# Optimization experiments

Hardware: AMD Instinct MI355X
Metric: run time of the kernel (lower is better)

## Reference

```python
import jax, jax.numpy as jnp
import numpy as np

EMBED = 1024
NUM_EXPERTS = 8
ACTIVE = 2
HIDDEN = 4 * EMBED


def setup_inputs() -> dict:
    key = jax.random.key(0)
    ks = jax.random.split(key, 7)
    B, T = 4, 1024
    s1 = 1.0 / np.sqrt(EMBED)
    s2 = 1.0 / np.sqrt(HIDDEN)
    return {
        "x": jax.random.normal(ks[0], (B, T, EMBED), dtype=jnp.float32),
        # stacked expert weights, layout [in, out] (torch Linear applies x @ W.T + b)
        "W1": jax.random.uniform(ks[1], (NUM_EXPERTS, EMBED, HIDDEN), jnp.float32, -s1, s1),
        "b1": jax.random.uniform(ks[2], (NUM_EXPERTS, HIDDEN), jnp.float32, -s1, s1),
        "W2": jax.random.uniform(ks[3], (NUM_EXPERTS, HIDDEN, EMBED), jnp.float32, -s2, s2),
        "b2": jax.random.uniform(ks[4], (NUM_EXPERTS, EMBED), jnp.float32, -s2, s2),
        "Wr": jax.random.uniform(ks[5], (EMBED, NUM_EXPERTS), jnp.float32, -s1, s1),
        "br": jax.random.uniform(ks[6], (NUM_EXPERTS,), jnp.float32, -s1, s1),
    }


def reference(x, W1, b1, W2, b2, Wr, br):
    # ---- router (TopkRouter) ----
    scores = x @ Wr + br                                  # [B,T,E]
    topk_scores, indices = jax.lax.top_k(scores, ACTIVE)  # [B,T,K]
    # mask = zeros scattered with topk scores at topk positions (others stay 0),
    # then softmax over ALL experts (faithful to the reference's quirky softmax).
    one_hot = jax.nn.one_hot(indices, NUM_EXPERTS, dtype=scores.dtype)  # [B,T,K,E]
    mask = jnp.einsum('btke,btk->bte', one_hot, topk_scores)            # [B,T,E]
    router_output = jax.nn.softmax(mask, axis=-1)                       # [B,T,E]

    # ---- dense all-experts FFN (Expert): relu(x@W1+b1)@W2+b2 per expert ----
    h = jax.nn.relu(jnp.einsum('btd,edh->bteh', x, W1) + b1)            # [B,T,E,H]
    expert_outputs = jnp.einsum('bteh,ehd->bted', h, W2) + b2           # [B,T,E,D]

    # ---- weighted combine ----
    return jnp.einsum('bte,bted->btd', router_output, expert_outputs)   # [B,T,D]
```

## Files before the change

kernel.cpp:

```cpp
#include <hip/hip_runtime.h>
#include <hip/hip_bf16.h>
#include <cstdint>
#include <cstddef>

#define EMBED  1024
#define NEXP   8
#define HIDDEN 4096
#define TOKENS 4096

typedef __attribute__((ext_vector_type(8))) short bf16x8;
typedef __attribute__((ext_vector_type(4))) float f32x4;
using bf16 = __hip_bfloat16;

__device__ __forceinline__ void gload_lds16(const void* g, void* l) {
    __builtin_amdgcn_global_load_lds((const __attribute__((address_space(1))) void*)g,
                                     (__attribute__((address_space(3))) void*)l,
                                     16, 0, 0);
}

__device__ __forceinline__ int swz(int b) { return b ^ (((b >> 7) & 7) << 4); }

__global__ void cvt_kernel(const float* __restrict__ in, bf16* __restrict__ out, size_t n) {
    size_t i = ((size_t)blockIdx.x * blockDim.x + threadIdx.x) * 4;
    if (i + 3 < n) {
        float4 v = *(const float4*)(in + i);
        out[i + 0] = __float2bfloat16(v.x);
        out[i + 1] = __float2bfloat16(v.y);
        out[i + 2] = __float2bfloat16(v.z);
        out[i + 3] = __float2bfloat16(v.w);
    }
}

__global__ void transpose_cvt(const float* __restrict__ in, bf16* __restrict__ out,
                              int K, int N, size_t in_estride, size_t out_eoff, int ldo) {
    const int e = blockIdx.z;
    const float* ine = in + (size_t)e * in_estride;
    bf16* oute = out + (size_t)e * out_eoff;
    __shared__ float tile[32][33];
    const int n0 = blockIdx.x * 32, k0 = blockIdx.y * 32;
    const int tx = threadIdx.x, ty = threadIdx.y;
    #pragma unroll
    for (int i = ty; i < 32; i += 8)
        tile[i][tx] = ine[(size_t)(k0 + i) * N + n0 + tx];
    __syncthreads();
    #pragma unroll
    for (int i = ty; i < 32; i += 8)
        oute[(size_t)(n0 + i) * ldo + k0 + tx] = __float2bfloat16(tile[tx][i]);
}

__global__ void router_kernel(const float* __restrict__ x, const float* __restrict__ Wr,
                              const float* __restrict__ br, float* __restrict__ w) {
    const int t = blockIdx.x;
    const int lane = threadIdx.x;
    const float* xt = x + (size_t)t * EMBED;
    float s[NEXP];
    #pragma unroll
    for (int e = 0; e < NEXP; e++) s[e] = 0.f;
    for (int k = lane; k < EMBED; k += 64) {
        const float xv = xt[k];
        const float* wrk = Wr + (size_t)k * NEXP;
        #pragma unroll
        for (int e = 0; e < NEXP; e++) s[e] = fmaf(xv, wrk[e], s[e]);
    }
    #pragma unroll
    for (int e = 0; e < NEXP; e++) {
        #pragma unroll
        for (int off = 32; off >= 1; off >>= 1)
            s[e] += __shfl_xor(s[e], off);
    }
    if (lane == 0) {
        float sc[NEXP];
        #pragma unroll
        for (int e = 0; e < NEXP; e++) sc[e] = s[e] + br[e];
        int i1 = 0; float m1 = sc[0];
        #pragma unroll
        for (int e = 1; e < NEXP; e++) if (sc[e] > m1) { m1 = sc[e]; i1 = e; }
        int i2 = -1; float m2 = -1e30f;
        #pragma unroll
        for (int e = 0; e < NEXP; e++) if (e != i1 && sc[e] > m2) { m2 = sc[e]; i2 = e; }
        const float mx = fmaxf(m1, 0.f);
        const float denom = 6.f * expf(0.f - mx) + expf(m1 - mx) + expf(m2 - mx);
        #pragma unroll
        for (int e = 0; e < NEXP; e++) {
            float v = (e == i1) ? m1 : ((e == i2) ? m2 : 0.f);
            w[(size_t)t * NEXP + e] = expf(v - mx) / denom;
        }
    }
}


#define BARX()  { __builtin_amdgcn_sched_barrier(0); __builtin_amdgcn_s_barrier(); __builtin_amdgcn_sched_barrier(0); }
#define LGKM0() { asm volatile("s_waitcnt lgkmcnt(0)" ::: "memory"); __builtin_amdgcn_sched_barrier(0); }

#define PIPE_PREAMBLE(Abase, Bbase, lda, ldb)                                        \
    __shared__ __align__(16) bf16 As[2][2][128 * 64];                                \
    __shared__ __align__(16) bf16 Bs[2][2][128 * 64];                                \
    const int tid = threadIdx.x;                                                     \
    const int lane = tid & 63, wid = tid >> 6;                                       \
    const int mhalf = wid >> 2, wB = wid & 3;                                        \
    const int nhalf = wB >> 1, nsub = wB & 1;                                        \
    const int wv_r = mhalf * 128, wv_c = wB * 64;                                    \
    f32x4 acc[8][4] = {};                                                            \
    int rowloc[2], colel[2];                                                         \
    _Pragma("unroll")                                                                \
    for (int j = 0; j < 2; j++) {                                                    \
        int bs = swz(tid * 16 + j * 8192);                                           \
        rowloc[j] = bs >> 7; colel[j] = (bs & 127) >> 1;                             \
    }                                                                                \
    const bf16* pA0 = (Abase) + (size_t)(brow + rowloc[0]) * (lda) + colel[0];       \
    const bf16* pA1 = (Abase) + (size_t)(brow + rowloc[1]) * (lda) + colel[1];       \
    const bf16* pB0 = (Bbase) + (size_t)(bcol + rowloc[0]) * (ldb) + colel[0];       \
    const bf16* pB1 = (Bbase) + (size_t)(bcol + rowloc[1]) * (ldb) + colel[1];       \
    const int fr = lane & 15, kb0 = (lane >> 4) * 16;                                \
    const int xm = (fr & 7) << 4;                                                    \
    const int baA0 = (fr * 128 + kb0) ^ xm, baA1 = (fr * 128 + kb0 + 64) ^ xm;       \
    const int brB = (nsub * 64 + fr) * 128;                                          \
    const int baB0 = (brB + kb0) ^ xm, baB1 = (brB + kb0 + 64) ^ xm;

#define STAGE_A(bi, h, koff, lda)                                                    \
    do {                                                                             \
        gload_lds16(pA0 + (size_t)(h) * 128 * (lda) + (koff), &As[bi][h][tid * 8]);  \
        gload_lds16(pA1 + (size_t)(h) * 128 * (lda) + (koff), &As[bi][h][tid * 8 + 4096]); \
    } while (0)
#define STAGE_B(bi, h, koff, ldb)                                                    \
    do {                                                                             \
        gload_lds16(pB0 + (size_t)(h) * 128 * (ldb) + (koff), &Bs[bi][h][tid * 8]);  \
        gload_lds16(pB1 + (size_t)(h) * 128 * (ldb) + (koff), &Bs[bi][h][tid * 8 + 4096]); \
    } while (0)

#define MFMA_Q(mh, nh)                                                               \
    __builtin_amdgcn_s_setprio(1);                                                   \
    _Pragma("unroll")                                                                \
    for (int mm = 0; mm < 4; mm++)                                                   \
        _Pragma("unroll")                                                            \
        for (int nn = 0; nn < 2; nn++) {                                             \
            acc[(mh)*4+mm][(nh)*2+nn] = __builtin_amdgcn_mfma_f32_16x16x32_bf16(     \
                a[(mh)*4+mm][0], b[(nh)*2+nn][0], acc[(mh)*4+mm][(nh)*2+nn], 0,0,0); \
            acc[(mh)*4+mm][(nh)*2+nn] = __builtin_amdgcn_mfma_f32_16x16x32_bf16(     \
                a[(mh)*4+mm][1], b[(nh)*2+nn][1], acc[(mh)*4+mm][(nh)*2+nn], 0,0,0); \
        }                                                                            \
    __builtin_amdgcn_s_setprio(0);

#define PIPE_KLOOP(NT, lda, ldb)                                                     \
    STAGE_A(0, 0, 0, lda); STAGE_A(0, 1, 0, lda);                                    \
    STAGE_B(0, 0, 0, ldb); STAGE_B(0, 1, 0, ldb);                                    \
    STAGE_A(1, 0, 64, lda); STAGE_A(1, 1, 64, lda);                                  \
    STAGE_B(1, 0, 64, ldb); STAGE_B(1, 1, 64, ldb);                                  \
    asm volatile("s_waitcnt vmcnt(8)" ::: "memory");                                 \
    BARX();                                                                          \
    for (int t = 0; t < (NT); ++t) {                                                 \
        const int bi = t & 1;                                                        \
        const bool st = (t + 2) < (NT);                                              \
        const size_t koff = (size_t)(t + 2) * 64;                                    \
        const char* Ah = (const char*)&As[bi][mhalf][0];                             \
        const char* Bh = (const char*)&Bs[bi][nhalf][0];                             \
        bf16x8 a[8][2], b[4][2];                                                     \
                             \
        _Pragma("unroll")                                                            \
        for (int m = 0; m < 4; m++) {                                                \
            a[m][0] = *(const bf16x8*)(Ah + baA0 + m * 2048);                        \
            a[m][1] = *(const bf16x8*)(Ah + baA1 + m * 2048);                        \
        }                                                                            \
        _Pragma("unroll")                                                            \
        for (int n = 0; n < 2; n++) {                                                \
            b[n][0] = *(const bf16x8*)(Bh + baB0 + n * 2048);                        \
            b[n][1] = *(const bf16x8*)(Bh + baB1 + n * 2048);                        \
        }                                                                            \
        BARX(); LGKM0();                                                             \
        MFMA_Q(0, 0)                                                                 \
        BARX();                                                                      \
                             \
        _Pragma("unroll")                                                            \
        for (int m = 4; m < 8; m++) {                                                \
            a[m][0] = *(const bf16x8*)(Ah + baA0 + m * 2048);                        \
            a[m][1] = *(const bf16x8*)(Ah + baA1 + m * 2048);                        \
        }                                                                            \
        _Pragma("unroll")                                                            \
        for (int n = 2; n < 4; n++) {                                                \
            b[n][0] = *(const bf16x8*)(Bh + baB0 + n * 2048);                        \
            b[n][1] = *(const bf16x8*)(Bh + baB1 + n * 2048);                        \
        }                                                                            \
        BARX(); LGKM0();                                                             \
        MFMA_Q(0, 1)                                                                 \
        BARX();                                                                      \
                \
        if (st) { STAGE_A(bi, 0, koff, lda); STAGE_A(bi, 1, koff, lda); }            \
        MFMA_Q(1, 0)                                                                 \
        BARX();                                                                      \
                      \
        if (st) { STAGE_B(bi, 0, koff, ldb); STAGE_B(bi, 1, koff, ldb); }            \
        MFMA_Q(1, 1)                                                                 \
        if (st) { asm volatile("s_waitcnt vmcnt(8)" ::: "memory"); }                 \
        else    { asm volatile("s_waitcnt vmcnt(0)" ::: "memory"); }                 \
        BARX();                                                                      \
    }

__global__ __launch_bounds__(512, 2) void gemm1(const bf16* __restrict__ A,
                                                const bf16* __restrict__ Bt,
                                                const float* __restrict__ b1,
                                                const float* __restrict__ rw,
                                                bf16* __restrict__ H) {
    const int e = blockIdx.z;
    const int brow = blockIdx.y * 256;
    const int bcol = blockIdx.x * 256;
    const bf16* Be = Bt + (size_t)e * HIDDEN * EMBED;
    bf16* He = H + (size_t)e * TOKENS * HIDDEN;

    PIPE_PREAMBLE(A, Be, EMBED, EMBED)
    PIPE_KLOOP(16, EMBED, EMBED)

    #pragma unroll
    for (int n = 0; n < 4; n++) {
        const int col = bcol + wv_c + n * 16 + fr;
        const float bias = b1[e * HIDDEN + col];
        #pragma unroll
        for (int m = 0; m < 8; m++) {
            const int rowb = brow + wv_r + m * 16 + (lane >> 4) * 4;
            #pragma unroll
            for (int j = 0; j < 4; j++) {
                const int row = rowb + j;
                float v = acc[m][n][j] + bias;
                v = fmaxf(v, 0.f) * rw[(size_t)row * NEXP + e];
                He[(size_t)row * HIDDEN + col] = __float2bfloat16(v);
            }
        }
    }
}

__global__ __launch_bounds__(512, 2) void gemm2(const bf16* __restrict__ A,
                                                const bf16* __restrict__ Bt,
                                                const float* __restrict__ b2,
                                                const float* __restrict__ rw,
                                                float* __restrict__ out) {
    const int e = blockIdx.z;
    const int brow = blockIdx.y * 256;
    const int bcol = blockIdx.x * 256;
    const bf16* Ae = A + (size_t)e * TOKENS * HIDDEN;
    const bf16* Be = Bt + (size_t)e * EMBED * HIDDEN;

    PIPE_PREAMBLE(Ae, Be, HIDDEN, HIDDEN)
    PIPE_KLOOP(64, HIDDEN, HIDDEN)

    #pragma unroll
    for (int n = 0; n < 4; n++) {
        const int col = bcol + wv_c + n * 16 + fr;
        #pragma unroll
        for (int m = 0; m < 8; m++) {
            const int rowb = brow + wv_r + m * 16 + (lane >> 4) * 4;
            #pragma unroll
            for (int j = 0; j < 4; j++) {
                const int row = rowb + j;
                float v = acc[m][n][j];
                if (e == 0) {
                    const float* wrow = rw + (size_t)row * NEXP;
                    float s = 0.f;
                    #pragma unroll
                    for (int ee = 0; ee < NEXP; ee++) s = fmaf(wrow[ee], b2[ee * EMBED + col], s);
                    v += s;
                }
                atomicAdd(out + (size_t)row * EMBED + col, v);
            }
        }
    }
}

extern "C" void kernel_launch(void* const* d_in, const int* in_sizes, int n_in,
                              void* d_out, int out_size, void* d_ws, size_t ws_size,
                              hipStream_t stream) {
    const float* x  = (const float*)d_in[0];
    const float* W1 = (const float*)d_in[1];
    const float* b1 = (const float*)d_in[2];
    const float* W2 = (const float*)d_in[3];
    const float* b2 = (const float*)d_in[4];
    const float* Wr = (const float*)d_in[5];
    const float* br = (const float*)d_in[6];
    float* out = (float*)d_out;

    uint8_t* ws = (uint8_t*)d_ws;
    size_t off = 0;
    auto walloc = [&](size_t bytes) -> void* {
        void* p = ws + off;
        off += (bytes + 255) & ~(size_t)255;
        return p;
    };
    float* rw  = (float*)walloc((size_t)TOKENS * NEXP * 4);
    bf16* xb   = (bf16*)walloc((size_t)TOKENS * EMBED * 2);
    bf16* w1t  = (bf16*)walloc((size_t)NEXP * HIDDEN * EMBED * 2);
    bf16* w2t  = (bf16*)walloc((size_t)NEXP * EMBED * HIDDEN * 2);
    bf16* hbuf = (bf16*)walloc((size_t)NEXP * TOKENS * HIDDEN * 2);

    hipMemsetAsync(d_out, 0, (size_t)out_size * sizeof(float), stream);

    cvt_kernel<<<4096, 256, 0, stream>>>(x, xb, (size_t)TOKENS * EMBED);

    dim3 tb(32, 8);
    transpose_cvt<<<dim3(HIDDEN / 32, EMBED / 32, NEXP), tb, 0, stream>>>(
        W1, w1t, EMBED, HIDDEN, (size_t)EMBED * HIDDEN, (size_t)HIDDEN * EMBED, EMBED);
    transpose_cvt<<<dim3(EMBED / 32, HIDDEN / 32, NEXP), tb, 0, stream>>>(
        W2, w2t, HIDDEN, EMBED, (size_t)HIDDEN * EMBED, (size_t)EMBED * HIDDEN, HIDDEN);

    router_kernel<<<TOKENS, 64, 0, stream>>>(x, Wr, br, rw);

    gemm1<<<dim3(HIDDEN / 256, TOKENS / 256, NEXP), 512, 0, stream>>>(xb, w1t, b1, rw, hbuf);
    gemm2<<<dim3(EMBED / 256, TOKENS / 256, NEXP), 512, 0, stream>>>(hbuf, w2t, b2, rw, out);
}
```

Before: 950.6 us.

## Replace gemm1 with simple 128x128 tile kernel and reorder gemm2 pipeline stages

```diff
diff --git a/kernel.cpp b/kernel.cpp
--- a/kernel.cpp
+++ b/kernel.cpp
@@ -84,6 +84,70 @@
         for (int e = 0; e < NEXP; e++) {
             float v = (e == i1) ? m1 : ((e == i2) ? m2 : 0.f);
             w[(size_t)t * NEXP + e] = expf(v - mx) / denom;
+        }
+    }
+}
+
+__global__ __launch_bounds__(256) void gemm1(const bf16* __restrict__ A,
+                                             const bf16* __restrict__ Bt,
+                                             const float* __restrict__ b1,
+                                             const float* __restrict__ rw,
+                                             bf16* __restrict__ H) {
+    const int e = blockIdx.z;
+    const int brow = blockIdx.y * 128;
+    const int bcol = blockIdx.x * 128;
+    const bf16* Be = Bt + (size_t)e * HIDDEN * EMBED;
+    bf16* He = H + (size_t)e * TOKENS * HIDDEN;
+    __shared__ __align__(16) bf16 As[128 * 32];
+    __shared__ __align__(16) bf16 Bs[128 * 32];
+    const int tid = threadIdx.x;
+    f32x4 acc[4][4] = {};
+
+    const int seg0 = tid, seg1 = tid + 256;
+    const int r0 = seg0 >> 2, c0 = seg0 & 3;
+    const int r1 = seg1 >> 2, c1 = seg1 & 3;
+    const bf16* ga0 = A + (size_t)(brow + r0) * EMBED + c0 * 8;
+    const bf16* ga1 = A + (size_t)(brow + r1) * EMBED + c1 * 8;
+    const bf16* gb0 = Be + (size_t)(bcol + r0) * EMBED + c0 * 8;
+    const bf16* gb1 = Be + (size_t)(bcol + r1) * EMBED + c1 * 8;
+
+    const int lane = tid & 63, wid = tid >> 6;
+    const int wv_r = (wid >> 1) * 64, wv_c = (wid & 1) * 64;
+    const int fr = lane & 15, kb = (lane >> 4) * 8;
+
+    for (int kt = 0; kt < EMBED; kt += 32) {
+        gload_lds16(ga0 + kt, As + seg0 * 8);
+        gload_lds16(ga1 + kt, As + seg1 * 8);
+        gload_lds16(gb0 + kt, Bs + seg0 * 8);
+        gload_lds16(gb1 + kt, Bs + seg1 * 8);
+        __syncthreads();
+        bf16x8 af[4], bfr[4];
+        #pragma unroll
+        for (int m = 0; m < 4; m++) af[m] = *(const bf16x8*)&As[(wv_r + m * 16 + fr) * 32 + kb];
+        #pragma unroll
+        for (int n = 0; n < 4; n++) bfr[n] = *(const bf16x8*)&Bs[(wv_c + n * 16 + fr) * 32 + kb];
+        #pragma unroll
+        for (int m = 0; m < 4; m++)
+            #pragma unroll
+            for (int n = 0; n < 4; n++)
+                acc[m][n] = __builtin_amdgcn_mfma_f32_16x16x32_bf16(af[m], bfr[n], acc[m][n], 0, 0, 0);
+        __syncthreads();
+    }
+
+    #pragma unroll
+    for (int n = 0; n < 4; n++) {
+        const int col = bcol + wv_c + n * 16 + fr;
+        const float bias = b1[e * HIDDEN + col];
+        #pragma unroll
+        for (int m = 0; m < 4; m++) {
+            const int rowb = brow + wv_r + m * 16 + (lane >> 4) * 4;
+            #pragma unroll
+            for (int j = 0; j < 4; j++) {
+                const int row = rowb + j;
+                float v = acc[m][n][j] + bias;
+                v = fmaxf(v, 0.f) * rw[(size_t)row * NEXP + e];
+                He[(size_t)row * HIDDEN + col] = __float2bfloat16(v);
+            }
         }
     }
 }
@@ -155,7 +219,7 @@
         const char* Ah = (const char*)&As[bi][mhalf][0];                             \
         const char* Bh = (const char*)&Bs[bi][nhalf][0];                             \
         bf16x8 a[8][2], b[4][2];                                                     \
-                             \
+                                        \
         _Pragma("unroll")                                                            \
         for (int m = 0; m < 4; m++) {                                                \
             a[m][0] = *(const bf16x8*)(Ah + baA0 + m * 2048);                        \
@@ -168,64 +232,32 @@
         }                                                                            \
         BARX(); LGKM0();                                                             \
         MFMA_Q(0, 0)                                                                 \
+             \
+        _Pragma("unroll")                                                            \
+        for (int n = 2; n < 4; n++) {                                                \
+            b[n][0] = *(const bf16x8*)(Bh + baB0 + n * 2048);                        \
+            b[n][1] = *(const bf16x8*)(Bh + baB1 + n * 2048);                        \
+        }                                                                            \
+        BARX(); LGKM0();                                                             \
+        MFMA_Q(0, 1)                                                                 \
         BARX();                                                                      \
-                             \
+           \
         _Pragma("unroll")                                                            \
         for (int m = 4; m < 8; m++) {                                                \
             a[m][0] = *(const bf16x8*)(Ah + baA0 + m * 2048);                        \
             a[m][1] = *(const bf16x8*)(Ah + baA1 + m * 2048);                        \
         }                                                                            \
-        _Pragma("unroll")                                                            \
-        for (int n = 2; n < 4; n++) {                                                \
-            b[n][0] = *(const bf16x8*)(Bh + baB0 + n * 2048);                        \
-            b[n][1] = *(const bf16x8*)(Bh + baB1 + n * 2048);                        \
-        }                                                                            \
+        if (st) { STAGE_B(bi, 0, koff, ldb); STAGE_B(bi, 1, koff, ldb); }            \
         BARX(); LGKM0();                                                             \
-        MFMA_Q(0, 1)                                                                 \
-        BARX();                                                                      \
-                \
-        if (st) { STAGE_A(bi, 0, koff, lda); STAGE_A(bi, 1, koff, lda); }            \
         MFMA_Q(1, 0)                                                                 \
         BARX();                                                                      \
-                      \
-        if (st) { STAGE_B(bi, 0, koff, ldb); STAGE_B(bi, 1, koff, ldb); }            \
+             \
+        if (st) { STAGE_A(bi, 0, koff, lda); STAGE_A(bi, 1, koff, lda); }            \
         MFMA_Q(1, 1)                                                                 \
         if (st) { asm volatile("s_waitcnt vmcnt(8)" ::: "memory"); }                 \
         else    { asm volatile("s_waitcnt vmcnt(0)" ::: "memory"); }                 \
         BARX();                                                                      \
     }
-
-__global__ __launch_bounds__(512, 2) void gemm1(const bf16* __restrict__ A,
-                                                const bf16* __restrict__ Bt,
-                                                const float* __restrict__ b1,
-                                                const float* __restrict__ rw,
-                                                bf16* __restrict__ H) {
-    const int e = blockIdx.z;
-    const int brow = blockIdx.y * 256;
-    const int bcol = blockIdx.x * 256;
-    const bf16* Be = Bt + (size_t)e * HIDDEN * EMBED;
-    bf16* He = H + (size_t)e * TOKENS * HIDDEN;
-
-    PIPE_PREAMBLE(A, Be, EMBED, EMBED)
-    PIPE_KLOOP(16, EMBED, EMBED)
-
-    #pragma unroll
-    for (int n = 0; n < 4; n++) {
-        const int col = bcol + wv_c + n * 16 + fr;
-        const float bias = b1[e * HIDDEN + col];
-        #pragma unroll
-        for (int m = 0; m < 8; m++) {
-            const int rowb = brow + wv_r + m * 16 + (lane >> 4) * 4;
-            #pragma unroll
-            for (int j = 0; j < 4; j++) {
-                const int row = rowb + j;
-                float v = acc[m][n][j] + bias;
-                v = fmaxf(v, 0.f) * rw[(size_t)row * NEXP + e];
-                He[(size_t)row * HIDDEN + col] = __float2bfloat16(v);
-            }
-        }
-    }
-}
 
 __global__ __launch_bounds__(512, 2) void gemm2(const bf16* __restrict__ A,
                                                 const bf16* __restrict__ Bt,
@@ -301,6 +333,6 @@
 
     router_kernel<<<TOKENS, 64, 0, stream>>>(x, Wr, br, rw);
 
-    gemm1<<<dim3(HIDDEN / 256, TOKENS / 256, NEXP), 512, 0, stream>>>(xb, w1t, b1, rw, hbuf);
+    gemm1<<<dim3(HIDDEN / 128, TOKENS / 128, NEXP), 256, 0, stream>>>(xb, w1t, b1, rw, hbuf);
     gemm2<<<dim3(EMBED / 256, TOKENS / 256, NEXP), 512, 0, stream>>>(hbuf, w2t, b2, rw, out);
 }
```

Result: no change. 941.5 us (-1.0%).

## Replace gemm2 fp32 atomics with per-expert-pair partials and a reduce kernel

Applied to the files above, without the earlier changes.

```diff
diff --git a/kernel.cpp b/kernel.cpp
--- a/kernel.cpp
+++ b/kernel.cpp
@@ -18,7 +18,7 @@
                                      16, 0, 0);
 }
 
-__device__ __forceinline__ int swz(int b) { return b ^ (((b >> 7) & 7) << 4); }
+__device__ __forceinline__ int swzB(int b) { return b ^ (((b >> 7) & 7) << 4); }
 
 __global__ void cvt_kernel(const float* __restrict__ in, bf16* __restrict__ out, size_t n) {
     size_t i = ((size_t)blockIdx.x * blockDim.x + threadIdx.x) * 4;
@@ -88,9 +88,40 @@
     }
 }
 
+__global__ __launch_bounds__(256) void reduce_kernel(const float* __restrict__ p,
+                                                     const float* __restrict__ rw,
+                                                     const float* __restrict__ b2,
+                                                     float* __restrict__ out) {
+    const int row = blockIdx.x;
+    const int c4 = threadIdx.x * 4;
+    const size_t S = (size_t)TOKENS * EMBED;
+    const float* pr = p + (size_t)row * EMBED + c4;
+    float4 v0 = *(const float4*)(pr);
+    float4 v1 = *(const float4*)(pr + S);
+    float4 v2 = *(const float4*)(pr + 2 * S);
+    float4 v3 = *(const float4*)(pr + 3 * S);
+    float4 v;
+    v.x = v0.x + v1.x + v2.x + v3.x;
+    v.y = v0.y + v1.y + v2.y + v3.y;
+    v.z = v0.z + v1.z + v2.z + v3.z;
+    v.w = v0.w + v1.w + v2.w + v3.w;
+    const float* wrow = rw + (size_t)row * NEXP;
+    #pragma unroll
+    for (int e = 0; e < NEXP; e++) {
+        const float we = wrow[e];
+        float4 bb = *(const float4*)(b2 + (size_t)e * EMBED + c4);
+        v.x = fmaf(we, bb.x, v.x);
+        v.y = fmaf(we, bb.y, v.y);
+        v.z = fmaf(we, bb.z, v.z);
+        v.w = fmaf(we, bb.w, v.w);
+    }
+    *(float4*)(out + (size_t)row * EMBED + c4) = v;
+}
 
 #define BARX()  { __builtin_amdgcn_sched_barrier(0); __builtin_amdgcn_s_barrier(); __builtin_amdgcn_sched_barrier(0); }
 #define LGKM0() { asm volatile("s_waitcnt lgkmcnt(0)" ::: "memory"); __builtin_amdgcn_sched_barrier(0); }
+
+#define KOFF(T, estride) ((size_t)((T) & 63) * 64 + (size_t)((T) >> 6) * (estride))
 
 #define PIPE_PREAMBLE(Abase, Bbase, lda, ldb)                                        \
     __shared__ __align__(16) bf16 As[2][2][128 * 64];                                \
@@ -104,7 +135,7 @@
     int rowloc[2], colel[2];                                                         \
     _Pragma("unroll")                                                                \
     for (int j = 0; j < 2; j++) {                                                    \
-        int bs = swz(tid * 16 + j * 8192);                                           \
+        int bs = swzB(tid * 16 + j * 8192);                                          \
         rowloc[j] = bs >> 7; colel[j] = (bs & 127) >> 1;                             \
     }                                                                                \
     const bf16* pA0 = (Abase) + (size_t)(brow + rowloc[0]) * (lda) + colel[0];       \
@@ -141,7 +172,7 @@
         }                                                                            \
     __builtin_amdgcn_s_setprio(0);
 
-#define PIPE_KLOOP(NT, lda, ldb)                                                     \
+#define PIPE_KLOOP(NT, lda, ldb, eA, eB)                                             \
     STAGE_A(0, 0, 0, lda); STAGE_A(0, 1, 0, lda);                                    \
     STAGE_B(0, 0, 0, ldb); STAGE_B(0, 1, 0, ldb);                                    \
     STAGE_A(1, 0, 64, lda); STAGE_A(1, 1, 64, lda);                                  \
@@ -151,11 +182,12 @@
     for (int t = 0; t < (NT); ++t) {                                                 \
         const int bi = t & 1;                                                        \
         const bool st = (t + 2) < (NT);                                              \
-        const size_t koff = (size_t)(t + 2) * 64;                                    \
+        const size_t koffA = KOFF(t + 2, eA);                                        \
+        const size_t koffB = KOFF(t + 2, eB);                                        \
         const char* Ah = (const char*)&As[bi][mhalf][0];                             \
         const char* Bh = (const char*)&Bs[bi][nhalf][0];                             \
         bf16x8 a[8][2], b[4][2];                                                     \
-                             \
+                                        \
         _Pragma("unroll")                                                            \
         for (int m = 0; m < 4; m++) {                                                \
             a[m][0] = *(const bf16x8*)(Ah + baA0 + m * 2048);                        \
@@ -168,27 +200,27 @@
         }                                                                            \
         BARX(); LGKM0();                                                             \
         MFMA_Q(0, 0)                                                                 \
+                                                   \
+        _Pragma("unroll")                                                            \
+        for (int n = 2; n < 4; n++) {                                                \
+            b[n][0] = *(const bf16x8*)(Bh + baB0 + n * 2048);                        \
+            b[n][1] = *(const bf16x8*)(Bh + baB1 + n * 2048);                        \
+        }                                                                            \
+        BARX(); LGKM0();                                                             \
+        MFMA_Q(0, 1)                                                                 \
         BARX();                                                                      \
-                             \
+                                     \
         _Pragma("unroll")                                                            \
         for (int m = 4; m < 8; m++) {                                                \
             a[m][0] = *(const bf16x8*)(Ah + baA0 + m * 2048);                        \
             a[m][1] = *(const bf16x8*)(Ah + baA1 + m * 2048);                        \
         }                                                                            \
-        _Pragma("unroll")                                                            \
-        for (int n = 2; n < 4; n++) {                                                \
-            b[n][0] = *(const bf16x8*)(Bh + baB0 + n * 2048);                        \
-            b[n][1] = *(const bf16x8*)(Bh + baB1 + n * 2048);                        \
-        }                                                                            \
+        if (st) { STAGE_B(bi, 0, koffB, ldb); STAGE_B(bi, 1, koffB, ldb); }          \
         BARX(); LGKM0();                                                             \
-        MFMA_Q(0, 1)                                                                 \
-        BARX();                                                                      \
-                \
-        if (st) { STAGE_A(bi, 0, koff, lda); STAGE_A(bi, 1, koff, lda); }            \
         MFMA_Q(1, 0)                                                                 \
         BARX();                                                                      \
-                      \
-        if (st) { STAGE_B(bi, 0, koff, ldb); STAGE_B(bi, 1, koff, ldb); }            \
+                       \
+        if (st) { STAGE_A(bi, 0, koffA, lda); STAGE_A(bi, 1, koffA, lda); }          \
         MFMA_Q(1, 1)                                                                 \
         if (st) { asm volatile("s_waitcnt vmcnt(8)" ::: "memory"); }                 \
         else    { asm volatile("s_waitcnt vmcnt(0)" ::: "memory"); }                 \
@@ -207,7 +239,7 @@
     bf16* He = H + (size_t)e * TOKENS * HIDDEN;
 
     PIPE_PREAMBLE(A, Be, EMBED, EMBED)
-    PIPE_KLOOP(16, EMBED, EMBED)
+    PIPE_KLOOP(16, EMBED, EMBED, (size_t)0, (size_t)0)
 
     #pragma unroll
     for (int n = 0; n < 4; n++) {
@@ -229,17 +261,18 @@
 
 __global__ __launch_bounds__(512, 2) void gemm2(const bf16* __restrict__ A,
                                                 const bf16* __restrict__ Bt,
-                                                const float* __restrict__ b2,
-                                                const float* __restrict__ rw,
-                                                float* __restrict__ out) {
-    const int e = blockIdx.z;
+                                                float* __restrict__ partials) {
+    const int kc = blockIdx.z;
     const int brow = blockIdx.y * 256;
     const int bcol = blockIdx.x * 256;
-    const bf16* Ae = A + (size_t)e * TOKENS * HIDDEN;
-    const bf16* Be = Bt + (size_t)e * EMBED * HIDDEN;
+    const size_t eA = (size_t)TOKENS * HIDDEN;
+    const size_t eB = (size_t)EMBED * HIDDEN;
+    const bf16* Ae = A + (size_t)(kc * 2) * eA;
+    const bf16* Be = Bt + (size_t)(kc * 2) * eB;
+    float* pout = partials + (size_t)kc * TOKENS * EMBED;
 
     PIPE_PREAMBLE(Ae, Be, HIDDEN, HIDDEN)
-    PIPE_KLOOP(64, HIDDEN, HIDDEN)
+    PIPE_KLOOP(128, HIDDEN, HIDDEN, eA, eB)
 
     #pragma unroll
     for (int n = 0; n < 4; n++) {
@@ -250,15 +283,7 @@
             #pragma unroll
             for (int j = 0; j < 4; j++) {
                 const int row = rowb + j;
-                float v = acc[m][n][j];
-                if (e == 0) {
-                    const float* wrow = rw + (size_t)row * NEXP;
-                    float s = 0.f;
-                    #pragma unroll
-                    for (int ee = 0; ee < NEXP; ee++) s = fmaf(wrow[ee], b2[ee * EMBED + col], s);
-                    v += s;
-                }
-                atomicAdd(out + (size_t)row * EMBED + col, v);
+                pout[(size_t)row * EMBED + col] = acc[m][n][j];
             }
         }
     }
@@ -288,8 +313,7 @@
     bf16* w1t  = (bf16*)walloc((size_t)NEXP * HIDDEN * EMBED * 2);
     bf16* w2t  = (bf16*)walloc((size_t)NEXP * EMBED * HIDDEN * 2);
     bf16* hbuf = (bf16*)walloc((size_t)NEXP * TOKENS * HIDDEN * 2);
-
-    hipMemsetAsync(d_out, 0, (size_t)out_size * sizeof(float), stream);
+    float* partials = (float*)w1t;
 
     cvt_kernel<<<4096, 256, 0, stream>>>(x, xb, (size_t)TOKENS * EMBED);
 
@@ -302,5 +326,6 @@
     router_kernel<<<TOKENS, 64, 0, stream>>>(x, Wr, br, rw);
 
     gemm1<<<dim3(HIDDEN / 256, TOKENS / 256, NEXP), 512, 0, stream>>>(xb, w1t, b1, rw, hbuf);
-    gemm2<<<dim3(EMBED / 256, TOKENS / 256, NEXP), 512, 0, stream>>>(hbuf, w2t, b2, rw, out);
-}
+    gemm2<<<dim3(EMBED / 256, TOKENS / 256, 4), 512, 0, stream>>>(hbuf, w2t, partials);
+    reduce_kernel<<<TOKENS, 256, 0, stream>>>(partials, rw, b2, out);
+}
```

Measured after the change: 813.2 us. -14.5%, faster.
